# Kernel optimization log

Hardware: AMD Instinct MI355X
Metric: run time of the kernel (lower is better)

## Reference

```python
import jax, jax.numpy as jnp
import numpy as np

N_NODES = 100000
N_EDGES = 800000
D = 64      # conv_dim == out_dim (skip connection)
H = 128     # conv hidden width


def _w(k, i, o):
    return jax.random.normal(k, (i, o), jnp.float32) * (1.0 / np.sqrt(i))


def setup_inputs() -> dict:
    key = jax.random.key(0)
    ks = jax.random.split(key, 40)
    inp = {
        "edge_feat": jax.random.normal(ks[0], (N_EDGES, D), jnp.float32),
        "node_feat": jax.random.normal(ks[1], (N_NODES, D), jnp.float32),
        "graph_attr": jax.random.normal(ks[2], (1, D), jnp.float32),
        "src": jax.random.randint(ks[3], (N_EDGES,), 0, N_NODES),
        "dst": jax.random.randint(ks[4], (N_EDGES,), 0, N_NODES),
        # pre-dense MLPs (dims=[64,64], Softplus, activate_last)
        "pre_edge_w": _w(ks[5], D, D), "pre_edge_b": jnp.zeros((D,), jnp.float32),
        "pre_node_w": _w(ks[6], D, D), "pre_node_b": jnp.zeros((D,), jnp.float32),
        "pre_attr_w": _w(ks[7], D, D), "pre_attr_b": jnp.zeros((D,), jnp.float32),
        # conv edge MLP: [4D, H, H, D]
        "edge_w0": _w(ks[8], 4 * D, H), "edge_b0": jnp.zeros((H,), jnp.float32),
        "edge_w1": _w(ks[9], H, H),     "edge_b1": jnp.zeros((H,), jnp.float32),
        "edge_w2": _w(ks[10], H, D),    "edge_b2": jnp.zeros((D,), jnp.float32),
        # conv node MLP: [3D, H, H, D]
        "node_w0": _w(ks[11], 3 * D, H), "node_b0": jnp.zeros((H,), jnp.float32),
        "node_w1": _w(ks[12], H, H),     "node_b1": jnp.zeros((H,), jnp.float32),
        "node_w2": _w(ks[13], H, D),     "node_b2": jnp.zeros((D,), jnp.float32),
        # conv attr MLP: [3D, H, H, D]
        "attr_w0": _w(ks[14], 3 * D, H), "attr_b0": jnp.zeros((H,), jnp.float32),
        "attr_w1": _w(ks[15], H, H),     "attr_b1": jnp.zeros((H,), jnp.float32),
        "attr_w2": _w(ks[16], H, D),     "attr_b2": jnp.zeros((D,), jnp.float32),
    }
    return inp


def _mlp(x, layers):
    # Linear + Softplus after every layer (activate_last=True)
    for w, b in layers:
        x = jax.nn.softplus(x @ w + b)
    return x


def reference(edge_feat, node_feat, graph_attr, src, dst,
              pre_edge_w, pre_edge_b, pre_node_w, pre_node_b, pre_attr_w, pre_attr_b,
              edge_w0, edge_b0, edge_w1, edge_b1, edge_w2, edge_b2,
              node_w0, node_b0, node_w1, node_b1, node_w2, node_b2,
              attr_w0, attr_b0, attr_w1, attr_b1, attr_w2, attr_b2):
    e_in, v_in, u_in = edge_feat, node_feat, graph_attr

    # pre-dense MLPs
    e = _mlp(edge_feat, [(pre_edge_w, pre_edge_b)])   # [E, D]
    v = _mlp(node_feat, [(pre_node_w, pre_node_b)])   # [N, D]
    u = _mlp(graph_attr, [(pre_attr_w, pre_attr_b)])  # [1, D]

    n_nodes = v.shape[0]

    # edge update: hstack([v_src, v_dst, e, u_broadcast]) -> edge MLP
    edge_in = jnp.concatenate(
        [v[src], v[dst], e, jnp.broadcast_to(u, (e.shape[0], u.shape[1]))], axis=1)  # [E, 4D]
    e_new = _mlp(edge_in, [(edge_w0, edge_b0), (edge_w1, edge_b1), (edge_w2, edge_b2)])  # [E, D]

    # node update: mean of incoming edge messages (segment-mean over dst)
    cnt = jax.ops.segment_sum(jnp.ones((e_new.shape[0], 1), e_new.dtype), dst,
                              num_segments=n_nodes)
    ve = jax.ops.segment_sum(e_new, dst, num_segments=n_nodes) / jnp.maximum(cnt, 1.0)
    node_in = jnp.concatenate(
        [v, ve, jnp.broadcast_to(u, (n_nodes, u.shape[1]))], axis=1)  # [N, 3D]
    v_new = _mlp(node_in, [(node_w0, node_b0), (node_w1, node_b1), (node_w2, node_b2)])  # [N, D]

    # attr update: mean readouts over edges and nodes
    ue = jnp.mean(e_new, axis=0, keepdims=True)  # [1, D]
    uv = jnp.mean(v_new, axis=0, keepdims=True)  # [1, D]
    attr_in = jnp.concatenate([u, ue, uv], axis=1)  # [1, 3D]
    u_new = _mlp(attr_in, [(attr_w0, attr_b0), (attr_w1, attr_b1), (attr_w2, attr_b2)])  # [1, D]

    # skip connections
    return (e_new + e_in, v_new + v_in, u_new + u_in)
```

## Files before the change

### kernel.cpp

```cpp
#include <hip/hip_runtime.h>
#include <cstddef>


typedef __attribute__((ext_vector_type(8))) short short8;
typedef __attribute__((ext_vector_type(4))) float f32x4;
typedef __attribute__((ext_vector_type(4))) unsigned int u32x4;
typedef __attribute__((ext_vector_type(2))) unsigned int u32x2;

__device__ __forceinline__ float sp(float x) {
    return fmaxf(x, 0.f) + __logf(1.f + __expf(-fabsf(x)));
}
__device__ __forceinline__ unsigned short f2bf(float x) {
    unsigned int u = __float_as_uint(x);
    u += 0x7fff + ((u >> 16) & 1);
    return (unsigned short)(u >> 16);
}
__device__ __forceinline__ unsigned int cvtpk(float lo, float hi) {
    unsigned int r;
    asm("v_cvt_pk_bf16_f32 %0, %1, %2" : "=v"(r) : "v"(lo), "v"(hi));
    return r;
}
__device__ __forceinline__ u32x4 pack8(f32x4 a, f32x4 b) {
    u32x4 r;
    r.x = cvtpk(a[0], a[1]); r.y = cvtpk(a[2], a[3]);
// ... 24 lines not shown
    else if (idx < 53248) { src = We2; K = 128; N = 64;  base = 45056; }
    else if (idx < 69632) { src = Wn0; K = 128; N = 128; base = 53248; }
    else if (idx < 86016) { src = Wn1; K = 128; N = 128; base = 69632; }
    else if (idx < 94208) { src = Wn2; K = 128; N = 64;  base = 86016; }
    else if (idx < 98304) { src = Wpn; K = 64;  N = 64;  base = 94208; }
    else return;
    int r = idx - base, n = r / K, k = r % K;
    out[idx] = f2bf(src[(size_t)k * N + n]);
}

__global__ __launch_bounds__(256) void pre_node_kernel(
    const float* __restrict__ nf, const unsigned short* __restrict__ WpnT,
    const float* __restrict__ b, unsigned short* __restrict__ vb, int N)
{
    __shared__ __align__(16) char lds[16384];
    const int t = threadIdx.x, w = t >> 6, l = t & 63;
    const int l15 = l & 15, l4 = l >> 4;
    const int n0 = blockIdx.x * 64;

#pragma unroll
    for (int rr = 0; rr < 2; ++rr) {
        int f = t + 256 * rr;
        int e = f >> 3, c = f & 7;
        int n = n0 + e; if (n >= N) n = N - 1;
        const float* p = nf + (size_t)n * 64 + c * 8;
        f32x4 x0 = *(const f32x4*)p, x1 = *(const f32x4*)(p + 4);
        *(u32x4*)(lds + swz(e, c, 128)) = pack8(x0, x1);
    }
    __syncthreads();
    {
        const int nr = w * 16;
        short8 A0 = *(const short8*)(WpnT + (nr + l15) * 64 + l4 * 8);
        short8 A1 = *(const short8*)(WpnT + (nr + l15) * 64 + 32 + l4 * 8);
        f32x4 bb = *(const f32x4*)(b + nr + l4 * 4);
        const int ochunk = (nr >> 3) + (l4 >> 1), obyte = (l4 & 1) * 8;
#pragma unroll
        for (int tt = 0; tt < 4; ++tt) {
            short8 b0 = *(const short8*)(lds + swz(tt * 16 + l15, l4, 128));
            short8 b1 = *(const short8*)(lds + swz(tt * 16 + l15, 4 + l4, 128));
            f32x4 acc = {0.f, 0.f, 0.f, 0.f};
            acc = mfma16(A0, b0, acc);
            acc = mfma16(A1, b1, acc);
            u32x2 p;
            p.x = cvtpk(sp(acc[0] + bb[0]), sp(acc[1] + bb[1]));
            p.y = cvtpk(sp(acc[2] + bb[2]), sp(acc[3] + bb[3]));
            *(u32x2*)(lds + 8192 + swz(tt * 16 + l15, ochunk, 128) + obyte) = p;
        }
    }
    __syncthreads();
#pragma unroll
    for (int rr = 0; rr < 2; ++rr) {
        int f = t + 256 * rr;
        int e = f >> 3, c = f & 7;
        int n = n0 + e;
        if (n < N) {
            u32x4 d = *(const u32x4*)(lds + 8192 + swz(e, c, 128));
            *(u32x4*)(vb + (size_t)n * 64 + c * 8) = d;
        }
    }
}

__global__ void pre_attr_kernel(
    const float* __restrict__ ga, const float* __restrict__ Wpa, const float* __restrict__ bpa,
    const float* __restrict__ eW0, const float* __restrict__ eb0,
    const float* __restrict__ nW0, const float* __restrict__ nb0,
    float* __restrict__ u, float* __restrict__ c0e, float* __restrict__ c0n)
{
    __shared__ float us[64];
    const int t = threadIdx.x;
    if (t < 64) {
        float acc = bpa[t];
        for (int k = 0; k < 64; ++k) acc += ga[k] * Wpa[k * 64 + t];
        float uu = sp(acc);
        us[t] = uu;
        u[t] = uu;
    }
    __syncthreads();
    if (t < 128) {
        float acc = eb0[t];
        for (int k = 0; k < 64; ++k) acc += us[k] * eW0[(192 + k) * 128 + t];
        c0e[t] = acc;
        float accn = nb0[t];
        for (int k = 0; k < 64; ++k) accn += us[k] * nW0[(128 + k) * 128 + t];
        c0n[t] = accn;
    }
}

__global__ __launch_bounds__(256) void cnt_kernel(
    const int* __restrict__ dst, int* __restrict__ cnt, int E)
{
    int i = blockIdx.x * 256 + threadIdx.x;
    if (i < E) atomicAdd(&cnt[dst[i]], 1);
}

__global__ __launch_bounds__(256) void scan1_kernel(
    const int* __restrict__ cnt, int* __restrict__ woff, int* __restrict__ bsum, int N)
{
    __shared__ int wsum[4];
    const int t = threadIdx.x, lane = t & 63, wv = t >> 6;
    const int i0 = blockIdx.x * 1024 + t * 4;
    int v0 = (i0 + 0 < N) ? cnt[i0 + 0] : 0;
    int v1 = (i0 + 1 < N) ? cnt[i0 + 1] : 0;
    int v2 = (i0 + 2 < N) ? cnt[i0 + 2] : 0;
    int v3 = (i0 + 3 < N) ? cnt[i0 + 3] : 0;
    int ts = v0 + v1 + v2 + v3;
    int sc = ts;
    for (int d = 1; d < 64; d <<= 1) {
        int up = __shfl_up(sc, d);
        if (lane >= d) sc += up;
    }
    if (lane == 63) wsum[wv] = sc;
    __syncthreads();
    int woffs = 0;
    for (int i = 0; i < wv; ++i) woffs += wsum[i];
    int ex = woffs + sc - ts;
    if (i0 + 0 < N) woff[i0 + 0] = ex;            ex += v0;
    if (i0 + 1 < N) woff[i0 + 1] = ex;            ex += v1;
    if (i0 + 2 < N) woff[i0 + 2] = ex;            ex += v2;
    if (i0 + 3 < N) woff[i0 + 3] = ex;
    if (t == 0) bsum[blockIdx.x] = wsum[0] + wsum[1] + wsum[2] + wsum[3];
}

__global__ void scan2_kernel(int* __restrict__ bsum, int nb)
{
    __shared__ int s[256];
    const int t = threadIdx.x;
    if (t < nb) s[t] = bsum[t];
    __syncthreads();
    if (t == 0) {
        int a = 0;
        for (int i = 0; i < nb; ++i) { int v = s[i]; s[i] = a; a += v; }
    }
    __syncthreads();
    if (t < nb) bsum[t] = s[t];
}

__global__ __launch_bounds__(256) void scan3_kernel(
    int* __restrict__ woff, int* __restrict__ wcur, const int* __restrict__ bsum, int N)
{
    const int base = blockIdx.x * 1024;
    const int add = bsum[blockIdx.x];
#pragma unroll
    for (int r = 0; r < 4; ++r) {
        int i = base + r * 256 + threadIdx.x;
        if (i < N) {
            int o = woff[i] + add;
            woff[i] = o;
            wcur[i] = o;
        }
    }
}

__global__ __launch_bounds__(256) void scatter_kernel(
    const int* __restrict__ dst, int* __restrict__ wcur, int* __restrict__ eidx, int E)
{
    int i = blockIdx.x * 256 + threadIdx.x;
    if (i < E) {
        int d = dst[i];
        int p = atomicAdd(&wcur[d], 1);
        eidx[p] = i;
    }
}

#define ELDS_X  0
#define ELDS_H  12288
#define ELDS_EF 12288

__global__ __launch_bounds__(256, 4) void edge_kernel(
    const float* __restrict__ ef, const unsigned short* __restrict__ vb,
    const int* __restrict__ src, const int* __restrict__ dst,
    const unsigned short* __restrict__ WpeT, const float* __restrict__ bpe,
    const unsigned short* __restrict__ W0T, const float* __restrict__ c0e,
    const unsigned short* __restrict__ W1T, const float* __restrict__ b1,
    const unsigned short* __restrict__ W2T, const float* __restrict__ b2,
    float* __restrict__ e_out, unsigned short* __restrict__ ebf)
{
    __shared__ __align__(16) char lds[20480];
    const int t = threadIdx.x;
    const int w = t >> 6, l = t & 63;
    const int l15 = l & 15, l4 = l >> 4;
    const int e0 = blockIdx.x * 32;

    f32x4 efr0, efr1;
    {
        int e = t >> 4, c = t & 15;
        efr0 = *(const f32x4*)(ef + (size_t)(e0 + e) * 64 + c * 4);
        u32x2 p;
        p.x = cvtpk(efr0[0], efr0[1]);
        p.y = cvtpk(efr0[2], efr0[3]);
        *(u32x2*)(lds + ELDS_EF + swz(e, c >> 1, 128) + (c & 1) * 8) = p;
        int f2 = t + 256;
        e = f2 >> 4; c = f2 & 15;
        efr1 = *(const f32x4*)(ef + (size_t)(e0 + e) * 64 + c * 4);
        p.x = cvtpk(efr1[0], efr1[1]);
        p.y = cvtpk(efr1[2], efr1[3]);
        *(u32x2*)(lds + ELDS_EF + swz(e, c >> 1, 128) + (c & 1) * 8) = p;
    }
#pragma unroll
    for (int rr = 0; rr < 2; ++rr) {
        int f = t + 256 * rr;
        int e = f >> 4, c = f & 15;
        int node = (c < 8) ? src[e0 + e] : dst[e0 + e];
        u32x4 d = *(const u32x4*)(vb + (size_t)node * 64 + (c & 7) * 8);
        *(u32x4*)(lds + ELDS_X + swz(e, c, 384)) = d;
    }
    __syncthreads();

    {
        const int nr = w * 16;
        short8 A0 = *(const short8*)(WpeT + (nr + l15) * 64 + l4 * 8);
        short8 A1 = *(const short8*)(WpeT + (nr + l15) * 64 + 32 + l4 * 8);
        f32x4 bb = *(const f32x4*)(bpe + nr + l4 * 4);
        const int ochunk = ((128 + nr) >> 3) + (l4 >> 1), obyte = (l4 & 1) * 8;
#pragma unroll
        for (int tt = 0; tt < 2; ++tt) {
            short8 b0 = *(const short8*)(lds + ELDS_EF + swz(tt * 16 + l15, l4, 128));
            short8 b1 = *(const short8*)(lds + ELDS_EF + swz(tt * 16 + l15, 4 + l4, 128));
            f32x4 acc = {0.f, 0.f, 0.f, 0.f};
            acc = mfma16(A0, b0, acc);
            acc = mfma16(A1, b1, acc);
            u32x2 p;
            p.x = cvtpk(sp(acc[0] + bb[0]), sp(acc[1] + bb[1]));
            p.y = cvtpk(sp(acc[2] + bb[2]), sp(acc[3] + bb[3]));
            *(u32x2*)(lds + ELDS_X + swz(tt * 16 + l15, ochunk, 384) + obyte) = p;
        }
    }
    __syncthreads();

    {
        const int nr0 = w * 32, nr1 = nr0 + 16;
        short8 A[2][6];
#pragma unroll
        for (int a = 0; a < 2; ++a)
#pragma unroll
            for (int ks = 0; ks < 6; ++ks)
                A[a][ks] = *(const short8*)(W0T + (nr0 + a * 16 + l15) * 192 + ks * 32 + l4 * 8);
        f32x4 bb0 = *(const f32x4*)(c0e + nr0 + l4 * 4);
        f32x4 bb1 = *(const f32x4*)(c0e + nr1 + l4 * 4);
        const int oc0 = (nr0 >> 3) + (l4 >> 1), oc1 = (nr1 >> 3) + (l4 >> 1);
        const int obyte = (l4 & 1) * 8;
#pragma unroll
        for (int tt = 0; tt < 2; ++tt) {
            f32x4 a0 = {0.f, 0.f, 0.f, 0.f}, a1 = {0.f, 0.f, 0.f, 0.f};
#pragma unroll
            for (int ks = 0; ks < 6; ++ks) {
                short8 b = *(const short8*)(lds + ELDS_X + swz(tt * 16 + l15, ks * 4 + l4, 384));
                a0 = mfma16(A[0][ks], b, a0);
                a1 = mfma16(A[1][ks], b, a1);
            }
            u32x2 p0, p1;
            p0.x = cvtpk(sp(a0[0] + bb0[0]), sp(a0[1] + bb0[1]));
            p0.y = cvtpk(sp(a0[2] + bb0[2]), sp(a0[3] + bb0[3]));
            p1.x = cvtpk(sp(a1[0] + bb1[0]), sp(a1[1] + bb1[1]));
            p1.y = cvtpk(sp(a1[2] + bb1[2]), sp(a1[3] + bb1[3]));
            *(u32x2*)(lds + ELDS_H + swz(tt * 16 + l15, oc0, 256) + obyte) = p0;
            *(u32x2*)(lds + ELDS_H + swz(tt * 16 + l15, oc1, 256) + obyte) = p1;
        }
    }
    __syncthreads();

    {
        const int nr0 = w * 32, nr1 = nr0 + 16;
        short8 A[2][4];
#pragma unroll
        for (int a = 0; a < 2; ++a)
#pragma unroll
            for (int ks = 0; ks < 4; ++ks)
                A[a][ks] = *(const short8*)(W1T + (nr0 + a * 16 + l15) * 128 + ks * 32 + l4 * 8);
        f32x4 bb0 = *(const f32x4*)(b1 + nr0 + l4 * 4);
        f32x4 bb1 = *(const f32x4*)(b1 + nr1 + l4 * 4);
        const int oc0 = (nr0 >> 3) + (l4 >> 1), oc1 = (nr1 >> 3) + (l4 >> 1);
        const int obyte = (l4 & 1) * 8;
#pragma unroll
        for (int tt = 0; tt < 2; ++tt) {
            f32x4 a0 = {0.f, 0.f, 0.f, 0.f}, a1 = {0.f, 0.f, 0.f, 0.f};
#pragma unroll
            for (int ks = 0; ks < 4; ++ks) {
                short8 b = *(const short8*)(lds + ELDS_H + swz(tt * 16 + l15, ks * 4 + l4, 256));
                a0 = mfma16(A[0][ks], b, a0);
                a1 = mfma16(A[1][ks], b, a1);
            }
            u32x2 p0, p1;
            p0.x = cvtpk(sp(a0[0] + bb0[0]), sp(a0[1] + bb0[1]));
            p0.y = cvtpk(sp(a0[2] + bb0[2]), sp(a0[3] + bb0[3]));
            p1.x = cvtpk(sp(a1[0] + bb1[0]), sp(a1[1] + bb1[1]));
            p1.y = cvtpk(sp(a1[2] + bb1[2]), sp(a1[3] + bb1[3]));
            *(u32x2*)(lds + ELDS_X + swz(tt * 16 + l15, oc0, 256) + obyte) = p0;
            *(u32x2*)(lds + ELDS_X + swz(tt * 16 + l15, oc1, 256) + obyte) = p1;
        }
    }
    __syncthreads();

    {
        const int nr = w * 16;
        short8 A[4];
#pragma unroll
        for (int ks = 0; ks < 4; ++ks)
            A[ks] = *(const short8*)(W2T + (nr + l15) * 128 + ks * 32 + l4 * 8);
        f32x4 bb = *(const f32x4*)(b2 + nr + l4 * 4);
        const int ochunk = (nr >> 2) + l4;
#pragma unroll
        for (int tt = 0; tt < 2; ++tt) {
            f32x4 acc = {0.f, 0.f, 0.f, 0.f};
#pragma unroll
            for (int ks = 0; ks < 4; ++ks) {
                short8 b = *(const short8*)(lds + ELDS_X + swz(tt * 16 + l15, ks * 4 + l4, 256));
                acc = mfma16(A[ks], b, acc);
            }
            f32x4 y = {sp(acc[0] + bb[0]), sp(acc[1] + bb[1]),
                       sp(acc[2] + bb[2]), sp(acc[3] + bb[3])};
            *(f32x4*)(lds + ELDS_H + swz(tt * 16 + l15, ochunk, 256)) = y;
        }
    }
    __syncthreads();

    {
        int e = t >> 4, c = t & 15;
        f32x4 en = *(const f32x4*)(lds + ELDS_H + swz(e, c, 256));
        *(f32x4*)(e_out + (size_t)(e0 + e) * 64 + c * 4) = en + efr0;
        if (ebf) {
            u32x2 pk;
            pk.x = cvtpk(en[0], en[1]);
            pk.y = cvtpk(en[2], en[3]);
            *(u32x2*)(ebf + (size_t)(e0 + e) * 64 + c * 4) = pk;
        }
        int f2 = t + 256;
        e = f2 >> 4; c = f2 & 15;
        en = *(const f32x4*)(lds + ELDS_H + swz(e, c, 256));
        *(f32x4*)(e_out + (size_t)(e0 + e) * 64 + c * 4) = en + efr1;
        if (ebf) {
            u32x2 pk;
            pk.x = cvtpk(en[0], en[1]);
            pk.y = cvtpk(en[2], en[3]);
            *(u32x2*)(ebf + (size_t)(e0 + e) * 64 + c * 4) = pk;
        }
    }
}

#define NLDS_X 0
#define NLDS_H 16384

__global__ __launch_bounds__(256, 3) void node_kernel(
    const float* __restrict__ nf, const unsigned short* __restrict__ vb,
    const int* __restrict__ cnt, const int* __restrict__ woff,
    const int* __restrict__ eidx,
    const unsigned short* __restrict__ ebf,
    const float* __restrict__ e_out_full, const float* __restrict__ ef_full,
    const unsigned short* __restrict__ W0T, const float* __restrict__ c0n,
    const unsigned short* __restrict__ W1T, const float* __restrict__ b1,
    const unsigned short* __restrict__ W2T, const float* __restrict__ b2,
    float* __restrict__ v_out, float* __restrict__ acc_e, float* __restrict__ acc_v,
    int N)
{
    __shared__ __align__(16) char lds[32768];
    const int t = threadIdx.x;
    const int w = t >> 6, l = t & 63;
    const int l15 = l & 15, l4 = l >> 4;
    const int n0 = blockIdx.x * 64;

#pragma unroll
    for (int rr = 0; rr < 2; ++rr) {
        int f = t + 256 * rr;
        int e = f >> 3, c = f & 7;
        int n = n0 + e; if (n >= N) n = N - 1;
        u32x4 d = *(const u32x4*)(vb + (size_t)n * 64 + c * 8);
        *(u32x4*)(lds + NLDS_X + swz(e, c, 256)) = d;
    }
    {
        const int e = t >> 2, p = t & 3;
        const int n = n0 + e;
        const bool valid = n < N;
        f32x4 a0 = {0,0,0,0}, a1 = {0,0,0,0}, a2 = {0,0,0,0}, a3 = {0,0,0,0};
        float rc = 0.f;
        if (valid) {
            const int off = woff[n], deg = cnt[n];
            rc = 1.f / fmaxf((float)deg, 1.f);
            if (ebf) {
                for (int j = 0; j < deg; ++j) {
                    int ed = eidx[off + j];
                    const unsigned short* row = ebf + (size_t)ed * 64 + p * 16;
                    u32x4 qa = *(const u32x4*)row;
                    u32x4 qb = *(const u32x4*)(row + 8);
                    a0[0] += bflo(qa.x); a0[1] += bfhi(qa.x);
                    a0[2] += bflo(qa.y); a0[3] += bfhi(qa.y);
                    a1[0] += bflo(qa.z); a1[1] += bfhi(qa.z);
                    a1[2] += bflo(qa.w); a1[3] += bfhi(qa.w);
                    a2[0] += bflo(qb.x); a2[1] += bfhi(qb.x);
                    a2[2] += bflo(qb.y); a2[3] += bfhi(qb.y);
                    a3[0] += bflo(qb.z); a3[1] += bfhi(qb.z);
                    a3[2] += bflo(qb.w); a3[3] += bfhi(qb.w);
                }
            } else {
                for (int j = 0; j < deg; ++j) {
                    int ed = eidx[off + j];
                    const float* ro = e_out_full + (size_t)ed * 64 + p * 16;
                    const float* ri = ef_full + (size_t)ed * 64 + p * 16;
                    a0 += *(const f32x4*)(ro + 0)  - *(const f32x4*)(ri + 0);
                    a1 += *(const f32x4*)(ro + 4)  - *(const f32x4*)(ri + 4);
                    a2 += *(const f32x4*)(ro + 8)  - *(const f32x4*)(ri + 8);
                    a3 += *(const f32x4*)(ro + 12) - *(const f32x4*)(ri + 12);
                }
            }
        }
        *(f32x4*)(lds + NLDS_H + swz(e, p * 4 + 0, 256)) = a0;
        *(f32x4*)(lds + NLDS_H + swz(e, p * 4 + 1, 256)) = a1;
        *(f32x4*)(lds + NLDS_H + swz(e, p * 4 + 2, 256)) = a2;
        *(f32x4*)(lds + NLDS_H + swz(e, p * 4 + 3, 256)) = a3;
        *(u32x4*)(lds + NLDS_X + swz(e, 8 + 2 * p, 256)) = pack8(a0 * rc, a1 * rc);
        *(u32x4*)(lds + NLDS_X + swz(e, 9 + 2 * p, 256)) = pack8(a2 * rc, a3 * rc);
    }
    __syncthreads();
    if (t < 64) {
        float s = 0.f;
        for (int row = 0; row < 64; ++row)
            s += *(const float*)(lds + NLDS_H + swz(row, t >> 2, 256) + (t & 3) * 4);
        atomicAdd(acc_e + t, s);
    }
    __syncthreads();

    {
        const int nr0 = w * 32, nr1 = nr0 + 16;
        short8 A[2][4];
#pragma unroll
        for (int a = 0; a < 2; ++a)
#pragma unroll
            for (int ks = 0; ks < 4; ++ks)
                A[a][ks] = *(const short8*)(W0T + (nr0 + a * 16 + l15) * 128 + ks * 32 + l4 * 8);
        f32x4 bb0 = *(const f32x4*)(c0n + nr0 + l4 * 4);
        f32x4 bb1 = *(const f32x4*)(c0n + nr1 + l4 * 4);
        const int oc0 = (nr0 >> 3) + (l4 >> 1), oc1 = (nr1 >> 3) + (l4 >> 1);
        const int obyte = (l4 & 1) * 8;
#pragma unroll
        for (int tt = 0; tt < 4; ++tt) {
            f32x4 a0 = {0.f, 0.f, 0.f, 0.f}, a1 = {0.f, 0.f, 0.f, 0.f};
#pragma unroll
            for (int ks = 0; ks < 4; ++ks) {
                short8 b = *(const short8*)(lds + NLDS_X + swz(tt * 16 + l15, ks * 4 + l4, 256));
                a0 = mfma16(A[0][ks], b, a0);
                a1 = mfma16(A[1][ks], b, a1);
            }
            u32x2 p0, p1;
            p0.x = cvtpk(sp(a0[0] + bb0[0]), sp(a0[1] + bb0[1]));
            p0.y = cvtpk(sp(a0[2] + bb0[2]), sp(a0[3] + bb0[3]));
            p1.x = cvtpk(sp(a1[0] + bb1[0]), sp(a1[1] + bb1[1]));
            p1.y = cvtpk(sp(a1[2] + bb1[2]), sp(a1[3] + bb1[3]));
            *(u32x2*)(lds + NLDS_H + swz(tt * 16 + l15, oc0, 256) + obyte) = p0;
            *(u32x2*)(lds + NLDS_H + swz(tt * 16 + l15, oc1, 256) + obyte) = p1;
        }
    }
    __syncthreads();

    {
        const int nr0 = w * 32, nr1 = nr0 + 16;
        short8 A[2][4];
#pragma unroll
        for (int a = 0; a < 2; ++a)
#pragma unroll
            for (int ks = 0; ks < 4; ++ks)
                A[a][ks] = *(const short8*)(W1T + (nr0 + a * 16 + l15) * 128 + ks * 32 + l4 * 8);
        f32x4 bb0 = *(const f32x4*)(b1 + nr0 + l4 * 4);
        f32x4 bb1 = *(const f32x4*)(b1 + nr1 + l4 * 4);
        const int oc0 = (nr0 >> 3) + (l4 >> 1), oc1 = (nr1 >> 3) + (l4 >> 1);
        const int obyte = (l4 & 1) * 8;
#pragma unroll
        for (int tt = 0; tt < 4; ++tt) {
            f32x4 a0 = {0.f, 0.f, 0.f, 0.f}, a1 = {0.f, 0.f, 0.f, 0.f};
#pragma unroll
            for (int ks = 0; ks < 4; ++ks) {
                short8 b = *(const short8*)(lds + NLDS_H + swz(tt * 16 + l15, ks * 4 + l4, 256));
                a0 = mfma16(A[0][ks], b, a0);
                a1 = mfma16(A[1][ks], b, a1);
            }
            u32x2 p0, p1;
            p0.x = cvtpk(sp(a0[0] + bb0[0]), sp(a0[1] + bb0[1]));
            p0.y = cvtpk(sp(a0[2] + bb0[2]), sp(a0[3] + bb0[3]));
            p1.x = cvtpk(sp(a1[0] + bb1[0]), sp(a1[1] + bb1[1]));
            p1.y = cvtpk(sp(a1[2] + bb1[2]), sp(a1[3] + bb1[3]));
            *(u32x2*)(lds + NLDS_X + swz(tt * 16 + l15, oc0, 256) + obyte) = p0;
            *(u32x2*)(lds + NLDS_X + swz(tt * 16 + l15, oc1, 256) + obyte) = p1;
        }
    }
    __syncthreads();

    {
        const int nr = w * 16;
        short8 A[4];
#pragma unroll
        for (int ks = 0; ks < 4; ++ks)
            A[ks] = *(const short8*)(W2T + (nr + l15) * 128 + ks * 32 + l4 * 8);
        f32x4 bb = *(const f32x4*)(b2 + nr + l4 * 4);
        const int ochunk = (nr >> 2) + l4;
#pragma unroll
        for (int tt = 0; tt < 4; ++tt) {
            f32x4 acc = {0.f, 0.f, 0.f, 0.f};
#pragma unroll
            for (int ks = 0; ks < 4; ++ks) {
                short8 b = *(const short8*)(lds + NLDS_X + swz(tt * 16 + l15, ks * 4 + l4, 256));
                acc = mfma16(A[ks], b, acc);
            }
            bool valid = (n0 + tt * 16 + l15) < N;
            f32x4 y;
            y[0] = valid ? sp(acc[0] + bb[0]) : 0.f;
            y[1] = valid ? sp(acc[1] + bb[1]) : 0.f;
            y[2] = valid ? sp(acc[2] + bb[2]) : 0.f;
            y[3] = valid ? sp(acc[3] + bb[3]) : 0.f;
            *(f32x4*)(lds + NLDS_H + swz(tt * 16 + l15, ochunk, 256)) = y;
        }
    }
    __syncthreads();

#pragma unroll
    for (int rr = 0; rr < 4; ++rr) {
        int f = t + 256 * rr;
        int e = f >> 4, c = f & 15;
        int n = n0 + e;
        if (n < N) {
            f32x4 vn = *(const f32x4*)(lds + NLDS_H + swz(e, c, 256));
            f32x4 x = *(const f32x4*)(nf + (size_t)n * 64 + c * 4);
            f32x4 o = vn + x;
            *(f32x4*)(v_out + (size_t)n * 64 + c * 4) = o;
        }
    }
    if (t < 64) {
        float s = 0.f;
        for (int row = 0; row < 64; ++row)
            s += *(const float*)(lds + NLDS_H + swz(row, t >> 2, 256) + (t & 3) * 4);
        atomicAdd(acc_v + t, s);
    }
}

__global__ void attr_kernel(
    const float* __restrict__ ga, const float* __restrict__ u,
    const float* __restrict__ acc_e, const float* __restrict__ acc_v,
    const float* __restrict__ W0, const float* __restrict__ b0,
    const float* __restrict__ W1, const float* __restrict__ b1,
    const float* __restrict__ W2, const float* __restrict__ b2,
    float* __restrict__ out_u, float Einv, float Ninv)
{
    __shared__ float ain[192];
    __shared__ float h0[128];
    __shared__ float h1[128];
    const int t = threadIdx.x;
    if (t < 64) {
        ain[t] = u[t];
        ain[64 + t] = acc_e[t] * Einv;
        ain[128 + t] = acc_v[t] * Ninv;
    }
    __syncthreads();
    if (t < 128) {
        float a = b0[t];
        for (int k = 0; k < 192; ++k) a += ain[k] * W0[k * 128 + t];
        h0[t] = sp(a);
    }
    __syncthreads();
    if (t < 128) {
        float a = b1[t];
        for (int k = 0; k < 128; ++k) a += h0[k] * W1[k * 128 + t];
        h1[t] = sp(a);
    }
    __syncthreads();
    if (t < 64) {
        float a = b2[t];
        for (int k = 0; k < 128; ++k) a += h1[k] * W2[k * 64 + t];
        out_u[t] = sp(a) + ga[t];
    }
}

extern "C" void kernel_launch(void* const* d_in, const int* in_sizes, int n_in,
                              void* d_out, int out_size, void* d_ws, size_t ws_size,
                              hipStream_t stream)
{
    const float* edge_feat = (const float*)d_in[0];
    const float* node_feat = (const float*)d_in[1];
    const float* graph_attr = (const float*)d_in[2];
    const int*   src = (const int*)d_in[3];
    const int*   dst = (const int*)d_in[4];
    const float* pre_edge_w = (const float*)d_in[5];
    const float* pre_edge_b = (const float*)d_in[6];
    const float* pre_node_w = (const float*)d_in[7];
    const float* pre_node_b = (const float*)d_in[8];
    const float* pre_attr_w = (const float*)d_in[9];
    const float* pre_attr_b = (const float*)d_in[10];
    const float* edge_w0 = (const float*)d_in[11];
    const float* edge_b0 = (const float*)d_in[12];
    const float* edge_w1 = (const float*)d_in[13];
    const float* edge_b1 = (const float*)d_in[14];
    const float* edge_w2 = (const float*)d_in[15];
    const float* edge_b2 = (const float*)d_in[16];
    const float* node_w0 = (const float*)d_in[17];
    const float* node_b0 = (const float*)d_in[18];
    const float* node_w1 = (const float*)d_in[19];
    const float* node_b1 = (const float*)d_in[20];
    const float* node_w2 = (const float*)d_in[21];
    const float* node_b2 = (const float*)d_in[22];
    const float* attr_w0 = (const float*)d_in[23];
    const float* attr_b0 = (const float*)d_in[24];
    const float* attr_w1 = (const float*)d_in[25];
    const float* attr_b1 = (const float*)d_in[26];
    const float* attr_w2 = (const float*)d_in[27];
    const float* attr_b2 = (const float*)d_in[28];

    const int E = in_sizes[0] / 64;
    const int N = in_sizes[1] / 64;
    const int NB = (N + 1023) / 1024;

    char* wsB = (char*)d_ws;
    size_t off = 0;
    auto alloc = [&](size_t bytes) { char* p = wsB + off; off += (bytes + 15) & ~(size_t)15; return p; };
    float* acc_e = (float*)alloc(64 * 4);
    float* acc_v = (float*)alloc(64 * 4);
    int*   cnt   = (int*)alloc((size_t)N * 4);
    float* u     = (float*)alloc(64 * 4);
    float* c0e   = (float*)alloc(128 * 4);
    float* c0n   = (float*)alloc(128 * 4);
    int*   bsum  = (int*)alloc((size_t)NB * 4);
    int*   woff  = (int*)alloc((size_t)N * 4);
    int*   wcur  = (int*)alloc((size_t)N * 4);
    int*   eidx  = (int*)alloc((size_t)E * 4);
    unsigned short* wT = (unsigned short*)alloc((size_t)98304 * 2);
    unsigned short* vb = (unsigned short*)alloc((size_t)N * 64 * 2);
    size_t off_no_ebf = off;
    unsigned short* ebf = (unsigned short*)alloc((size_t)E * 64 * 2);
    const bool use_ebf = (off <= ws_size);
    if (!use_ebf) { ebf = nullptr; off = off_no_ebf; }

    unsigned short* WpeT = wT;
    unsigned short* We0T = wT + 4096;
    unsigned short* We1T = wT + 28672;
    unsigned short* We2T = wT + 45056;
    unsigned short* Wn0T = wT + 53248;
    unsigned short* Wn1T = wT + 69632;
    unsigned short* Wn2T = wT + 86016;
    unsigned short* WpnT = wT + 94208;

    float* e_out = (float*)d_out;
    float* v_out = e_out + (size_t)E * 64;
    float* u_out = v_out + (size_t)N * 64;

    hipMemsetAsync(acc_e, 0, (size_t)(128 + N) * 4, stream);

    wprep<<<384, 256, 0, stream>>>(pre_edge_w, edge_w0, edge_w1, edge_w2,
                                   node_w0, node_w1, node_w2, pre_node_w, wT);
    pre_node_kernel<<<(N + 63) / 64, 256, 0, stream>>>(node_feat, WpnT, pre_node_b, vb, N);
    pre_attr_kernel<<<1, 128, 0, stream>>>(graph_attr, pre_attr_w, pre_attr_b,
                                           edge_w0, edge_b0, node_w0, node_b0,
                                           u, c0e, c0n);
    cnt_kernel<<<(E + 255) / 256, 256, 0, stream>>>(dst, cnt, E);
    scan1_kernel<<<NB, 256, 0, stream>>>(cnt, woff, bsum, N);
    scan2_kernel<<<1, 256, 0, stream>>>(bsum, NB);
    scan3_kernel<<<NB, 256, 0, stream>>>(woff, wcur, bsum, N);
    scatter_kernel<<<(E + 255) / 256, 256, 0, stream>>>(dst, wcur, eidx, E);
    edge_kernel<<<E / 32, 256, 0, stream>>>(
        edge_feat, vb, src, dst,
        WpeT, pre_edge_b, We0T, c0e, We1T, edge_b1, We2T, edge_b2,
        e_out, ebf);
    node_kernel<<<(N + 63) / 64, 256, 0, stream>>>(
        node_feat, vb, cnt, woff, eidx, ebf, e_out, edge_feat,
        Wn0T, c0n, Wn1T, node_b1, Wn2T, node_b2,
        v_out, acc_e, acc_v, N);
    attr_kernel<<<1, 128, 0, stream>>>(
        graph_attr, u, acc_e, acc_v,
        attr_w0, attr_b0, attr_w1, attr_b1, attr_w2, attr_b2,
        u_out, 1.f / (float)E, 1.f / (float)N);
}
```

Before: 625.3 us.

## Write bf16 edge messages in dst-sorted order and restructure edge layer-0 loop

The scatter step now records each edge's CSR slot, and the edge kernel writes its bf16 message copy directly to that slot. The node kernel can then stream contiguous rows instead of gathering through eidx. The layer-0 GEMM in the edge kernel is reorganised to load weights in two K-halves and compute both 16-row tiles together, aiming to cut register pressure; launch bounds rise from 4 to 5 blocks per SM. The cost is an extra E-sized int array plus scattered bf16 writes from the edge kernel. The a11 bias line also contains an odd `bb0[0]*0.f` term.

Result: no change. 630.1 us (+0.8%).

```diff
diff --git a/kernel.cpp b/kernel.cpp
--- a/kernel.cpp
+++ b/kernel.cpp
@@ -200,13 +200,15 @@
 }
 
 __global__ __launch_bounds__(256) void scatter_kernel(
-    const int* __restrict__ dst, int* __restrict__ wcur, int* __restrict__ eidx, int E)
+    const int* __restrict__ dst, int* __restrict__ wcur,
+    int* __restrict__ eidx, int* __restrict__ slot, int E)
 {
     int i = blockIdx.x * 256 + threadIdx.x;
     if (i < E) {
         int d = dst[i];
         int p = atomicAdd(&wcur[d], 1);
         eidx[p] = i;
+        slot[i] = p;
     }
 }
 
@@ -214,9 +216,10 @@
 #define ELDS_H  12288
 #define ELDS_EF 12288
 
-__global__ __launch_bounds__(256, 4) void edge_kernel(
+__global__ __launch_bounds__(256, 5) void edge_kernel(
     const float* __restrict__ ef, const unsigned short* __restrict__ vb,
     const int* __restrict__ src, const int* __restrict__ dst,
+    const int* __restrict__ slot,
     const unsigned short* __restrict__ WpeT, const float* __restrict__ bpe,
     const unsigned short* __restrict__ W0T, const float* __restrict__ c0e,
     const unsigned short* __restrict__ W1T, const float* __restrict__ b1,
@@ -277,33 +280,42 @@
 
     {
         const int nr0 = w * 32, nr1 = nr0 + 16;
-        short8 A[2][6];
-#pragma unroll
-        for (int a = 0; a < 2; ++a)
-#pragma unroll
-            for (int ks = 0; ks < 6; ++ks)
-                A[a][ks] = *(const short8*)(W0T + (nr0 + a * 16 + l15) * 192 + ks * 32 + l4 * 8);
+        f32x4 a00 = {0.f,0.f,0.f,0.f}, a01 = a00, a10 = a00, a11 = a00;
+#pragma unroll
+        for (int kh = 0; kh < 2; ++kh) {
+            short8 A0[3], A1[3];
+#pragma unroll
+            for (int k3 = 0; k3 < 3; ++k3) {
+                A0[k3] = *(const short8*)(W0T + (nr0 + l15) * 192 + (kh * 3 + k3) * 32 + l4 * 8);
+                A1[k3] = *(const short8*)(W0T + (nr1 + l15) * 192 + (kh * 3 + k3) * 32 + l4 * 8);
+            }
+#pragma unroll
+            for (int k3 = 0; k3 < 3; ++k3) {
+                short8 b0 = *(const short8*)(lds + ELDS_X + swz(l15,      (kh * 3 + k3) * 4 + l4, 384));
+                short8 b1 = *(const short8*)(lds + ELDS_X + swz(16 + l15, (kh * 3 + k3) * 4 + l4, 384));
+                a00 = mfma16(A0[k3], b0, a00);
+                a01 = mfma16(A1[k3], b0, a01);
+                a10 = mfma16(A0[k3], b1, a10);
+                a11 = mfma16(A1[k3], b1, a11);
+            }
+        }
         f32x4 bb0 = *(const f32x4*)(c0e + nr0 + l4 * 4);
         f32x4 bb1 = *(const f32x4*)(c0e + nr1 + l4 * 4);
         const int oc0 = (nr0 >> 3) + (l4 >> 1), oc1 = (nr1 >> 3) + (l4 >> 1);
         const int obyte = (l4 & 1) * 8;
-#pragma unroll
-        for (int tt = 0; tt < 2; ++tt) {
-            f32x4 a0 = {0.f, 0.f, 0.f, 0.f}, a1 = {0.f, 0.f, 0.f, 0.f};
-#pragma unroll
-            for (int ks = 0; ks < 6; ++ks) {
-                short8 b = *(const short8*)(lds + ELDS_X + swz(tt * 16 + l15, ks * 4 + l4, 384));
-                a0 = mfma16(A[0][ks], b, a0);
-                a1 = mfma16(A[1][ks], b, a1);
-            }
-            u32x2 p0, p1;
-            p0.x = cvtpk(sp(a0[0] + bb0[0]), sp(a0[1] + bb0[1]));
-            p0.y = cvtpk(sp(a0[2] + bb0[2]), sp(a0[3] + bb0[3]));
-            p1.x = cvtpk(sp(a1[0] + bb1[0]), sp(a1[1] + bb1[1]));
-            p1.y = cvtpk(sp(a1[2] + bb1[2]), sp(a1[3] + bb1[3]));
-            *(u32x2*)(lds + ELDS_H + swz(tt * 16 + l15, oc0, 256) + obyte) = p0;
-            *(u32x2*)(lds + ELDS_H + swz(tt * 16 + l15, oc1, 256) + obyte) = p1;
-        }
+        u32x2 p;
+        p.x = cvtpk(sp(a00[0] + bb0[0]), sp(a00[1] + bb0[1]));
+        p.y = cvtpk(sp(a00[2] + bb0[2]), sp(a00[3] + bb0[3]));
+        *(u32x2*)(lds + ELDS_H + swz(l15, oc0, 256) + obyte) = p;
+        p.x = cvtpk(sp(a01[0] + bb1[0]), sp(a01[1] + bb1[1]));
+        p.y = cvtpk(sp(a01[2] + bb1[2]), sp(a01[3] + bb1[3]));
+        *(u32x2*)(lds + ELDS_H + swz(l15, oc1, 256) + obyte) = p;
+        p.x = cvtpk(sp(a10[0] + bb0[0]), sp(a10[1] + bb0[1]));
+        p.y = cvtpk(sp(a10[2] + bb0[2]), sp(a10[3] + bb0[3]));
+        *(u32x2*)(lds + ELDS_H + swz(16 + l15, oc0, 256) + obyte) = p;
+        p.x = cvtpk(sp(a11[0] + bb0 [0]*0.f + bb1[0]), sp(a11[1] + bb1[1]));
+        p.y = cvtpk(sp(a11[2] + bb1[2]), sp(a11[3] + bb1[3]));
+        *(u32x2*)(lds + ELDS_H + swz(16 + l15, oc1, 256) + obyte) = p;
     }
     __syncthreads();
 
@@ -367,20 +379,22 @@
         f32x4 en = *(const f32x4*)(lds + ELDS_H + swz(e, c, 256));
         *(f32x4*)(e_out + (size_t)(e0 + e) * 64 + c * 4) = en + efr0;
         if (ebf) {
+            int sl = slot[e0 + e];
             u32x2 pk;
             pk.x = cvtpk(en[0], en[1]);
             pk.y = cvtpk(en[2], en[3]);
-            *(u32x2*)(ebf + (size_t)(e0 + e) * 64 + c * 4) = pk;
+            *(u32x2*)(ebf + (size_t)sl * 64 + c * 4) = pk;
         }
         int f2 = t + 256;
         e = f2 >> 4; c = f2 & 15;
         en = *(const f32x4*)(lds + ELDS_H + swz(e, c, 256));
         *(f32x4*)(e_out + (size_t)(e0 + e) * 64 + c * 4) = en + efr1;
         if (ebf) {
+            int sl = slot[e0 + e];
             u32x2 pk;
             pk.x = cvtpk(en[0], en[1]);
             pk.y = cvtpk(en[2], en[3]);
-            *(u32x2*)(ebf + (size_t)(e0 + e) * 64 + c * 4) = pk;
+            *(u32x2*)(ebf + (size_t)sl * 64 + c * 4) = pk;
         }
     }
 }
@@ -424,11 +438,11 @@
             const int off = woff[n], deg = cnt[n];
             rc = 1.f / fmaxf((float)deg, 1.f);
             if (ebf) {
+                const unsigned short* base = ebf + (size_t)off * 64 + p * 16;
                 for (int j = 0; j < deg; ++j) {
-                    int ed = eidx[off + j];
-                    const unsigned short* row = ebf + (size_t)ed * 64 + p * 16;
-                    u32x4 qa = *(const u32x4*)row;
-                    u32x4 qb = *(const u32x4*)(row + 8);
+                    u32x4 qa = *(const u32x4*)(base);
+                    u32x4 qb = *(const u32x4*)(base + 8);
+                    base += 64;
                     a0[0] += bflo(qa.x); a0[1] += bfhi(qa.x);
                     a0[2] += bflo(qa.y); a0[3] += bfhi(qa.y);
                     a1[0] += bflo(qa.z); a1[1] += bfhi(qa.z);
@@ -665,6 +679,7 @@
     int*   woff  = (int*)alloc((size_t)N * 4);
     int*   wcur  = (int*)alloc((size_t)N * 4);
     int*   eidx  = (int*)alloc((size_t)E * 4);
+    int*   slot  = (int*)alloc((size_t)E * 4);
     unsigned short* wT = (unsigned short*)alloc((size_t)98304 * 2);
     unsigned short* vb = (unsigned short*)alloc((size_t)N * 64 * 2);
     size_t off_no_ebf = off;
@@ -697,9 +712,9 @@
     scan1_kernel<<<NB, 256, 0, stream>>>(cnt, woff, bsum, N);
     scan2_kernel<<<1, 256, 0, stream>>>(bsum, NB);
     scan3_kernel<<<NB, 256, 0, stream>>>(woff, wcur, bsum, N);
-    scatter_kernel<<<(E + 255) / 256, 256, 0, stream>>>(dst, wcur, eidx, E);
+    scatter_kernel<<<(E + 255) / 256, 256, 0, stream>>>(dst, wcur, eidx, slot, E);
     edge_kernel<<<E / 32, 256, 0, stream>>>(
-        edge_feat, vb, src, dst,
+        edge_feat, vb, src, dst, slot,
         WpeT, pre_edge_b, We0T, c0e, We1T, edge_b1, We2T, edge_b2,
         e_out, ebf);
     node_kernel<<<(N + 63) / 64, 256, 0, stream>>>(
```

## Make edge kernel persistent with register prefetch and write edge messages dst-sorted

Applied to the files above, without the earlier changes.

The edge kernel becomes persistent: a fixed grid of 1536 blocks strides over 32-edge tiles. Each block prefetches the next tile's indices, edge features and gathered node rows into registers while the current tile's MLP layers run, which hides gather latency. The scatter pass also records each edge's position in dst-sorted order. The bf16 edge messages are written at that position, so the node kernel reads them contiguously instead of through eidx. The costs are one extra slot array, scattered bf16 writes in the edge kernel, and higher register pressure from holding the prefetched data.

New measurement: 816.6 us. 1.31x slower.

```diff
diff --git a/kernel.cpp b/kernel.cpp
--- a/kernel.cpp
+++ b/kernel.cpp
@@ -200,13 +200,15 @@
 }
 
 __global__ __launch_bounds__(256) void scatter_kernel(
-    const int* __restrict__ dst, int* __restrict__ wcur, int* __restrict__ eidx, int E)
+    const int* __restrict__ dst, int* __restrict__ wcur,
+    int* __restrict__ eidx, int* __restrict__ slot, int E)
 {
     int i = blockIdx.x * 256 + threadIdx.x;
     if (i < E) {
         int d = dst[i];
         int p = atomicAdd(&wcur[d], 1);
         eidx[p] = i;
+        slot[i] = p;
     }
 }
 
@@ -217,171 +219,190 @@
 __global__ __launch_bounds__(256, 4) void edge_kernel(
     const float* __restrict__ ef, const unsigned short* __restrict__ vb,
     const int* __restrict__ src, const int* __restrict__ dst,
+    const int* __restrict__ slot,
     const unsigned short* __restrict__ WpeT, const float* __restrict__ bpe,
     const unsigned short* __restrict__ W0T, const float* __restrict__ c0e,
     const unsigned short* __restrict__ W1T, const float* __restrict__ b1,
     const unsigned short* __restrict__ W2T, const float* __restrict__ b2,
-    float* __restrict__ e_out, unsigned short* __restrict__ ebf)
+    float* __restrict__ e_out, unsigned short* __restrict__ ebf, int T)
 {
     __shared__ __align__(16) char lds[20480];
     const int t = threadIdx.x;
     const int w = t >> 6, l = t & 63;
     const int l15 = l & 15, l4 = l >> 4;
-    const int e0 = blockIdx.x * 32;
-
-    f32x4 efr0, efr1;
+    const int G = gridDim.x;
+
+    const int eA = t >> 4,        cA = t & 15;
+    const int eB = (t + 256) >> 4, cB = (t + 256) & 15;
+
+    int tile = blockIdx.x;
+    f32x4 s_ef0, s_ef1; u32x4 s_vg0, s_vg1; int s_n0, s_n1, s_sl0, s_sl1;
     {
-        int e = t >> 4, c = t & 15;
-        efr0 = *(const f32x4*)(ef + (size_t)(e0 + e) * 64 + c * 4);
-        u32x2 p;
-        p.x = cvtpk(efr0[0], efr0[1]);
-        p.y = cvtpk(efr0[2], efr0[3]);
-        *(u32x2*)(lds + ELDS_EF + swz(e, c >> 1, 128) + (c & 1) * 8) = p;
-        int f2 = t + 256;
-        e = f2 >> 4; c = f2 & 15;
-        efr1 = *(const f32x4*)(ef + (size_t)(e0 + e) * 64 + c * 4);
-        p.x = cvtpk(efr1[0], efr1[1]);
-        p.y = cvtpk(efr1[2], efr1[3]);
-        *(u32x2*)(lds + ELDS_EF + swz(e, c >> 1, 128) + (c & 1) * 8) = p;
-    }
-#pragma unroll
-    for (int rr = 0; rr < 2; ++rr) {
-        int f = t + 256 * rr;
-        int e = f >> 4, c = f & 15;
-        int node = (c < 8) ? src[e0 + e] : dst[e0 + e];
-        u32x4 d = *(const u32x4*)(vb + (size_t)node * 64 + (c & 7) * 8);
-        *(u32x4*)(lds + ELDS_X + swz(e, c, 384)) = d;
-    }
-    __syncthreads();
-
-    {
-        const int nr = w * 16;
-        short8 A0 = *(const short8*)(WpeT + (nr + l15) * 64 + l4 * 8);
-        short8 A1 = *(const short8*)(WpeT + (nr + l15) * 64 + 32 + l4 * 8);
-        f32x4 bb = *(const f32x4*)(bpe + nr + l4 * 4);
-        const int ochunk = ((128 + nr) >> 3) + (l4 >> 1), obyte = (l4 & 1) * 8;
-#pragma unroll
-        for (int tt = 0; tt < 2; ++tt) {
-            short8 b0 = *(const short8*)(lds + ELDS_EF + swz(tt * 16 + l15, l4, 128));
-            short8 b1 = *(const short8*)(lds + ELDS_EF + swz(tt * 16 + l15, 4 + l4, 128));
-            f32x4 acc = {0.f, 0.f, 0.f, 0.f};
-            acc = mfma16(A0, b0, acc);
-            acc = mfma16(A1, b1, acc);
+        const int e0 = tile * 32;
+        s_n0 = (cA < 8) ? src[e0 + eA] : dst[e0 + eA];
+        s_n1 = (cB < 8) ? src[e0 + eB] : dst[e0 + eB];
+        s_sl0 = slot[e0 + eA];
+        s_sl1 = slot[e0 + eB];
+        s_ef0 = *(const f32x4*)(ef + (size_t)(e0 + eA) * 64 + cA * 4);
+        s_ef1 = *(const f32x4*)(ef + (size_t)(e0 + eB) * 64 + cB * 4);
+        s_vg0 = *(const u32x4*)(vb + (size_t)s_n0 * 64 + (cA & 7) * 8);
+        s_vg1 = *(const u32x4*)(vb + (size_t)s_n1 * 64 + (cB & 7) * 8);
+    }
+
+    for (; tile < T; tile += G) {
+        const int e0 = tile * 32;
+        const f32x4 efr0 = s_ef0, efr1 = s_ef1;
+        const int sl0 = s_sl0, sl1 = s_sl1;
+
+        {
             u32x2 p;
-            p.x = cvtpk(sp(acc[0] + bb[0]), sp(acc[1] + bb[1]));
-            p.y = cvtpk(sp(acc[2] + bb[2]), sp(acc[3] + bb[3]));
-            *(u32x2*)(lds + ELDS_X + swz(tt * 16 + l15, ochunk, 384) + obyte) = p;
-        }
-    }
-    __syncthreads();
-
-    {
-        const int nr0 = w * 32, nr1 = nr0 + 16;
-        short8 A[2][6];
-#pragma unroll
-        for (int a = 0; a < 2; ++a)
-#pragma unroll
-            for (int ks = 0; ks < 6; ++ks)
-                A[a][ks] = *(const short8*)(W0T + (nr0 + a * 16 + l15) * 192 + ks * 32 + l4 * 8);
-        f32x4 bb0 = *(const f32x4*)(c0e + nr0 + l4 * 4);
-        f32x4 bb1 = *(const f32x4*)(c0e + nr1 + l4 * 4);
-        const int oc0 = (nr0 >> 3) + (l4 >> 1), oc1 = (nr1 >> 3) + (l4 >> 1);
-        const int obyte = (l4 & 1) * 8;
-#pragma unroll
-        for (int tt = 0; tt < 2; ++tt) {
-            f32x4 a0 = {0.f, 0.f, 0.f, 0.f}, a1 = {0.f, 0.f, 0.f, 0.f};
-#pragma unroll
-            for (int ks = 0; ks < 6; ++ks) {
-                short8 b = *(const short8*)(lds + ELDS_X + swz(tt * 16 + l15, ks * 4 + l4, 384));
-                a0 = mfma16(A[0][ks], b, a0);
-                a1 = mfma16(A[1][ks], b, a1);
-            }
-            u32x2 p0, p1;
-            p0.x = cvtpk(sp(a0[0] + bb0[0]), sp(a0[1] + bb0[1]));
-            p0.y = cvtpk(sp(a0[2] + bb0[2]), sp(a0[3] + bb0[3]));
-            p1.x = cvtpk(sp(a1[0] + bb1[0]), sp(a1[1] + bb1[1]));
-            p1.y = cvtpk(sp(a1[2] + bb1[2]), sp(a1[3] + bb1[3]));
-            *(u32x2*)(lds + ELDS_H + swz(tt * 16 + l15, oc0, 256) + obyte) = p0;
-            *(u32x2*)(lds + ELDS_H + swz(tt * 16 + l15, oc1, 256) + obyte) = p1;
-        }
-    }
-    __syncthreads();
-
-    {
-        const int nr0 = w * 32, nr1 = nr0 + 16;
-        short8 A[2][4];
-#pragma unroll
-        for (int a = 0; a < 2; ++a)
+            p.x = cvtpk(efr0[0], efr0[1]); p.y = cvtpk(efr0[2], efr0[3]);
+            *(u32x2*)(lds + ELDS_EF + swz(eA, cA >> 1, 128) + (cA & 1) * 8) = p;
+            p.x = cvtpk(efr1[0], efr1[1]); p.y = cvtpk(efr1[2], efr1[3]);
+            *(u32x2*)(lds + ELDS_EF + swz(eB, cB >> 1, 128) + (cB & 1) * 8) = p;
+            *(u32x4*)(lds + ELDS_X + swz(eA, cA, 384)) = s_vg0;
+            *(u32x4*)(lds + ELDS_X + swz(eB, cB, 384)) = s_vg1;
+        }
+        const int ntile = tile + G;
+        const int ne0 = (ntile < T) ? ntile * 32 : 0;
+        s_n0 = (cA < 8) ? src[ne0 + eA] : dst[ne0 + eA];
+        s_n1 = (cB < 8) ? src[ne0 + eB] : dst[ne0 + eB];
+        s_sl0 = slot[ne0 + eA];
+        s_sl1 = slot[ne0 + eB];
+        __syncthreads();
+
+        {
+            const int nr = w * 16;
+            short8 A0 = *(const short8*)(WpeT + (nr + l15) * 64 + l4 * 8);
+            short8 A1 = *(const short8*)(WpeT + (nr + l15) * 64 + 32 + l4 * 8);
+            f32x4 bb = *(const f32x4*)(bpe + nr + l4 * 4);
+            const int ochunk = ((128 + nr) >> 3) + (l4 >> 1), obyte = (l4 & 1) * 8;
+#pragma unroll
+            for (int tt = 0; tt < 2; ++tt) {
+                short8 b0 = *(const short8*)(lds + ELDS_EF + swz(tt * 16 + l15, l4, 128));
+                short8 b1 = *(const short8*)(lds + ELDS_EF + swz(tt * 16 + l15, 4 + l4, 128));
+                f32x4 acc = {0.f, 0.f, 0.f, 0.f};
+                acc = mfma16(A0, b0, acc);
+                acc = mfma16(A1, b1, acc);
+                u32x2 p;
+                p.x = cvtpk(sp(acc[0] + bb[0]), sp(acc[1] + bb[1]));
+                p.y = cvtpk(sp(acc[2] + bb[2]), sp(acc[3] + bb[3]));
+                *(u32x2*)(lds + ELDS_X + swz(tt * 16 + l15, ochunk, 384) + obyte) = p;
+            }
+        }
+        __syncthreads();
+
+        s_ef0 = *(const f32x4*)(ef + (size_t)(ne0 + eA) * 64 + cA * 4);
+        s_ef1 = *(const f32x4*)(ef + (size_t)(ne0 + eB) * 64 + cB * 4);
+        s_vg0 = *(const u32x4*)(vb + (size_t)s_n0 * 64 + (cA & 7) * 8);
+        s_vg1 = *(const u32x4*)(vb + (size_t)s_n1 * 64 + (cB & 7) * 8);
+
+        {
+            const int nr0 = w * 32, nr1 = nr0 + 16;
+            short8 A[2][6];
+#pragma unroll
+            for (int a = 0; a < 2; ++a)
+#pragma unroll
+                for (int ks = 0; ks < 6; ++ks)
+                    A[a][ks] = *(const short8*)(W0T + (nr0 + a * 16 + l15) * 192 + ks * 32 + l4 * 8);
+            f32x4 bb0 = *(const f32x4*)(c0e + nr0 + l4 * 4);
+            f32x4 bb1 = *(const f32x4*)(c0e + nr1 + l4 * 4);
+            const int oc0 = (nr0 >> 3) + (l4 >> 1), oc1 = (nr1 >> 3) + (l4 >> 1);
+            const int obyte = (l4 & 1) * 8;
+#pragma unroll
+            for (int tt = 0; tt < 2; ++tt) {
+                f32x4 a0 = {0.f, 0.f, 0.f, 0.f}, a1 = {0.f, 0.f, 0.f, 0.f};
+#pragma unroll
+                for (int ks = 0; ks < 6; ++ks) {
+                    short8 b = *(const short8*)(lds + ELDS_X + swz(tt * 16 + l15, ks * 4 + l4, 384));
+                    a0 = mfma16(A[0][ks], b, a0);
+                    a1 = mfma16(A[1][ks], b, a1);
+                }
+                u32x2 p0, p1;
+                p0.x = cvtpk(sp(a0[0] + bb0[0]), sp(a0[1] + bb0[1]));
+                p0.y = cvtpk(sp(a0[2] + bb0[2]), sp(a0[3] + bb0[3]));
+                p1.x = cvtpk(sp(a1[0] + bb1[0]), sp(a1[1] + bb1[1]));
+                p1.y = cvtpk(sp(a1[2] + bb1[2]), sp(a1[3] + bb1[3]));
+                *(u32x2*)(lds + ELDS_H + swz(tt * 16 + l15, oc0, 256) + obyte) = p0;
+                *(u32x2*)(lds + ELDS_H + swz(tt * 16 + l15, oc1, 256) + obyte) = p1;
+            }
+        }
+        __syncthreads();
+
+        {
+            const int nr0 = w * 32, nr1 = nr0 + 16;
+            short8 A[2][4];
+#pragma unroll
+            for (int a = 0; a < 2; ++a)
+#pragma unroll
+                for (int ks = 0; ks < 4; ++ks)
+                    A[a][ks] = *(const short8*)(W1T + (nr0 + a * 16 + l15) * 128 + ks * 32 + l4 * 8);
+            f32x4 bb0 = *(const f32x4*)(b1 + nr0 + l4 * 4);
+            f32x4 bb1 = *(const f32x4*)(b1 + nr1 + l4 * 4);
+            const int oc0 = (nr0 >> 3) + (l4 >> 1), oc1 = (nr1 >> 3) + (l4 >> 1);
+            const int obyte = (l4 & 1) * 8;
+#pragma unroll
+            for (int tt = 0; tt < 2; ++tt) {
+                f32x4 a0 = {0.f, 0.f, 0.f, 0.f}, a1 = {0.f, 0.f, 0.f, 0.f};
+#pragma unroll
+                for (int ks = 0; ks < 4; ++ks) {
+                    short8 b = *(const short8*)(lds + ELDS_H + swz(tt * 16 + l15, ks * 4 + l4, 256));
+                    a0 = mfma16(A[0][ks], b, a0);
+                    a1 = mfma16(A[1][ks], b, a1);
+                }
+                u32x2 p0, p1;
+                p0.x = cvtpk(sp(a0[0] + bb0[0]), sp(a0[1] + bb0[1]));
+                p0.y = cvtpk(sp(a0[2] + bb0[2]), sp(a0[3] + bb0[3]));
+                p1.x = cvtpk(sp(a1[0] + bb1[0]), sp(a1[1] + bb1[1]));
+                p1.y = cvtpk(sp(a1[2] + bb1[2]), sp(a1[3] + bb1[3]));
+                *(u32x2*)(lds + ELDS_X + swz(tt * 16 + l15, oc0, 256) + obyte) = p0;
+                *(u32x2*)(lds + ELDS_X + swz(tt * 16 + l15, oc1, 256) + obyte) = p1;
+            }
+        }
+        __syncthreads();
+
+        {
+            const int nr = w * 16;
+            short8 A[4];
 #pragma unroll
             for (int ks = 0; ks < 4; ++ks)
-                A[a][ks] = *(const short8*)(W1T + (nr0 + a * 16 + l15) * 128 + ks * 32 + l4 * 8);
-        f32x4 bb0 = *(const f32x4*)(b1 + nr0 + l4 * 4);
-        f32x4 bb1 = *(const f32x4*)(b1 + nr1 + l4 * 4);
-        const int oc0 = (nr0 >> 3) + (l4 >> 1), oc1 = (nr1 >> 3) + (l4 >> 1);
-        const int obyte = (l4 & 1) * 8;
-#pragma unroll
-        for (int tt = 0; tt < 2; ++tt) {
-            f32x4 a0 = {0.f, 0.f, 0.f, 0.f}, a1 = {0.f, 0.f, 0.f, 0.f};
-#pragma unroll
-            for (int ks = 0; ks < 4; ++ks) {
-                short8 b = *(const short8*)(lds + ELDS_H + swz(tt * 16 + l15, ks * 4 + l4, 256));
-                a0 = mfma16(A[0][ks], b, a0);
-                a1 = mfma16(A[1][ks], b, a1);
-            }
-            u32x2 p0, p1;
-            p0.x = cvtpk(sp(a0[0] + bb0[0]), sp(a0[1] + bb0[1]));
-            p0.y = cvtpk(sp(a0[2] + bb0[2]), sp(a0[3] + bb0[3]));
-            p1.x = cvtpk(sp(a1[0] + bb1[0]), sp(a1[1] + bb1[1]));
-            p1.y = cvtpk(sp(a1[2] + bb1[2]), sp(a1[3] + bb1[3]));
-            *(u32x2*)(lds + ELDS_X + swz(tt * 16 + l15, oc0, 256) + obyte) = p0;
-            *(u32x2*)(lds + ELDS_X + swz(tt * 16 + l15, oc1, 256) + obyte) = p1;
-        }
-    }
-    __syncthreads();
-
-    {
-        const int nr = w * 16;
-        short8 A[4];
-#pragma unroll
-        for (int ks = 0; ks < 4; ++ks)
-            A[ks] = *(const short8*)(W2T + (nr + l15) * 128 + ks * 32 + l4 * 8);
-        f32x4 bb = *(const f32x4*)(b2 + nr + l4 * 4);
-        const int ochunk = (nr >> 2) + l4;
-#pragma unroll
-        for (int tt = 0; tt < 2; ++tt) {
-            f32x4 acc = {0.f, 0.f, 0.f, 0.f};
-#pragma unroll
-            for (int ks = 0; ks < 4; ++ks) {
-                short8 b = *(const short8*)(lds + ELDS_X + swz(tt * 16 + l15, ks * 4 + l4, 256));
-                acc = mfma16(A[ks], b, acc);
-            }
-            f32x4 y = {sp(acc[0] + bb[0]), sp(acc[1] + bb[1]),
-                       sp(acc[2] + bb[2]), sp(acc[3] + bb[3])};
-            *(f32x4*)(lds + ELDS_H + swz(tt * 16 + l15, ochunk, 256)) = y;
-        }
-    }
-    __syncthreads();
-
-    {
-        int e = t >> 4, c = t & 15;
-        f32x4 en = *(const f32x4*)(lds + ELDS_H + swz(e, c, 256));
-        *(f32x4*)(e_out + (size_t)(e0 + e) * 64 + c * 4) = en + efr0;
-        if (ebf) {
-            u32x2 pk;
-            pk.x = cvtpk(en[0], en[1]);
-            pk.y = cvtpk(en[2], en[3]);
-            *(u32x2*)(ebf + (size_t)(e0 + e) * 64 + c * 4) = pk;
-        }
-        int f2 = t + 256;
-        e = f2 >> 4; c = f2 & 15;
-        en = *(const f32x4*)(lds + ELDS_H + swz(e, c, 256));
-        *(f32x4*)(e_out + (size_t)(e0 + e) * 64 + c * 4) = en + efr1;
-        if (ebf) {
-            u32x2 pk;
-            pk.x = cvtpk(en[0], en[1]);
-            pk.y = cvtpk(en[2], en[3]);
-            *(u32x2*)(ebf + (size_t)(e0 + e) * 64 + c * 4) = pk;
-        }
+                A[ks] = *(const short8*)(W2T + (nr + l15) * 128 + ks * 32 + l4 * 8);
+            f32x4 bb = *(const f32x4*)(b2 + nr + l4 * 4);
+            const int ochunk = (nr >> 2) + l4;
+#pragma unroll
+            for (int tt = 0; tt < 2; ++tt) {
+                f32x4 acc = {0.f, 0.f, 0.f, 0.f};
+#pragma unroll
+                for (int ks = 0; ks < 4; ++ks) {
+                    short8 b = *(const short8*)(lds + ELDS_X + swz(tt * 16 + l15, ks * 4 + l4, 256));
+                    acc = mfma16(A[ks], b, acc);
+                }
+                f32x4 y = {sp(acc[0] + bb[0]), sp(acc[1] + bb[1]),
+                           sp(acc[2] + bb[2]), sp(acc[3] + bb[3])};
+                *(f32x4*)(lds + ELDS_H + swz(tt * 16 + l15, ochunk, 256)) = y;
+            }
+        }
+        __syncthreads();
+
+        {
+            f32x4 en = *(const f32x4*)(lds + ELDS_H + swz(eA, cA, 256));
+            *(f32x4*)(e_out + (size_t)(e0 + eA) * 64 + cA * 4) = en + efr0;
+            if (ebf) {
+                u32x2 pk;
+                pk.x = cvtpk(en[0], en[1]);
+                pk.y = cvtpk(en[2], en[3]);
+                *(u32x2*)(ebf + (size_t)sl0 * 64 + cA * 4) = pk;
+            }
+            en = *(const f32x4*)(lds + ELDS_H + swz(eB, cB, 256));
+            *(f32x4*)(e_out + (size_t)(e0 + eB) * 64 + cB * 4) = en + efr1;
+            if (ebf) {
+                u32x2 pk;
+                pk.x = cvtpk(en[0], en[1]);
+                pk.y = cvtpk(en[2], en[3]);
+                *(u32x2*)(ebf + (size_t)sl1 * 64 + cB * 4) = pk;
+            }
+        }
+        __syncthreads();
     }
 }
 
@@ -424,11 +445,11 @@
             const int off = woff[n], deg = cnt[n];
             rc = 1.f / fmaxf((float)deg, 1.f);
             if (ebf) {
+                const unsigned short* base = ebf + (size_t)off * 64 + p * 16;
                 for (int j = 0; j < deg; ++j) {
-                    int ed = eidx[off + j];
-                    const unsigned short* row = ebf + (size_t)ed * 64 + p * 16;
-                    u32x4 qa = *(const u32x4*)row;
-                    u32x4 qb = *(const u32x4*)(row + 8);
+                    u32x4 qa = *(const u32x4*)(base);
+                    u32x4 qb = *(const u32x4*)(base + 8);
+                    base += 64;
                     a0[0] += bflo(qa.x); a0[1] += bfhi(qa.x);
                     a0[2] += bflo(qa.y); a0[3] += bfhi(qa.y);
                     a1[0] += bflo(qa.z); a1[1] += bfhi(qa.z);
@@ -651,6 +672,7 @@
     const int E = in_sizes[0] / 64;
     const int N = in_sizes[1] / 64;
     const int NB = (N + 1023) / 1024;
+    const int T = E / 32;
 
     char* wsB = (char*)d_ws;
     size_t off = 0;
@@ -665,6 +687,7 @@
     int*   woff  = (int*)alloc((size_t)N * 4);
     int*   wcur  = (int*)alloc((size_t)N * 4);
     int*   eidx  = (int*)alloc((size_t)E * 4);
+    int*   slot  = (int*)alloc((size_t)E * 4);
     unsigned short* wT = (unsigned short*)alloc((size_t)98304 * 2);
     unsigned short* vb = (unsigned short*)alloc((size_t)N * 64 * 2);
     size_t off_no_ebf = off;
@@ -697,11 +720,15 @@
     scan1_kernel<<<NB, 256, 0, stream>>>(cnt, woff, bsum, N);
     scan2_kernel<<<1, 256, 0, stream>>>(bsum, NB);
     scan3_kernel<<<NB, 256, 0, stream>>>(woff, wcur, bsum, N);
-    scatter_kernel<<<(E + 255) / 256, 256, 0, stream>>>(dst, wcur, eidx, E);
-    edge_kernel<<<E / 32, 256, 0, stream>>>(
-        edge_feat, vb, src, dst,
-        WpeT, pre_edge_b, We0T, c0e, We1T, edge_b1, We2T, edge_b2,
-        e_out, ebf);
+    scatter_kernel<<<(E + 255) / 256, 256, 0, stream>>>(dst, wcur, eidx, slot, E);
+    {
+        int G = 1536;
+        if (G > T) G = T;
+        edge_kernel<<<G, 256, 0, stream>>>(
+            edge_feat, vb, src, dst, slot,
+            WpeT, pre_edge_b, We0T, c0e, We1T, edge_b1, We2T, edge_b2,
+            e_out, ebf, T);
+    }
     node_kernel<<<(N + 63) / 64, 256, 0, stream>>>(
         node_feat, vb, cnt, woff, eidx, ebf, e_out, edge_feat,
         Wn0T, c0n, Wn1T, node_b1, Wn2T, node_b2,
```
